# Kernel tuning notes

Measured on AMD Instinct MI355X. Metric: run time of the kernel, lower is better.

## Reference

```python
import jax, jax.numpy as jnp
import numpy as np

# Dimensions: B batch, V variables per sample, VT table rows, F feature, E embed_dim,
# NH healpix adjacency width. N6/N5/N4 grid sizes per zoom; PF fine patch points.
B, V, VT, F, E, NH = 2, 4, 4, 128, 128, 7
N6, N5, N4 = 196608, 49152, 12288
PF = 32768
P5, P4 = PF // 4, PF // 16   # coarse patch sizes
O5, O4 = 4, 16               # fine points per coarse point (4**(zoom - zoom_proc))
BIG = 1e10
EPS = 1e-20


def setup_inputs() -> dict:
    key = jax.random.key(0)
    ks = jax.random.split(key, 13)
    return {
        "table6": jax.random.normal(ks[0], (VT, N6, F), jnp.float32) * 0.02,
        "table5": jax.random.normal(ks[1], (VT, N5, F), jnp.float32) * 0.02,
        "table4": jax.random.normal(ks[2], (VT, N4, F), jnp.float32) * 0.02,
        "W": jax.random.normal(ks[3], (F, E), jnp.float32) / np.float32(np.sqrt(F)),
        "b": jnp.zeros((E,), jnp.float32),
        "rel_dists5": jax.random.uniform(ks[4], (B, P5, O5, NH), jnp.float32, 0.01, 1.0),
        "rel_dists4": jax.random.uniform(ks[5], (B, P4, O4, NH), jnp.float32, 0.01, 1.0),
        "mask5": (jax.random.uniform(ks[6], (B, P5, NH)) < 0.05).astype(jnp.float32),
        "mask4": (jax.random.uniform(ks[7], (B, P4, NH)) < 0.05).astype(jnp.float32),
        "var_indices": jax.random.randint(ks[8], (B, V), 0, VT),
        "idx6": jax.random.randint(ks[9], (B, PF), 0, N6),
        "nh_idx5": jax.random.randint(ks[10], (B, P5 * NH), 0, N5),
        "nh_idx4": jax.random.randint(ks[11], (B, P4 * NH), 0, N4),
    }


def _gather(table, var_idx, idx):
    # Fused get_embeddings_from_var_idx + get_patch / get_patch_nh:
    # out[b, v, p, f] = table[var_idx[b, v], idx[b, p], f]  -> [B, V, P, F]
    return table[var_idx[:, :, None], idx[:, None, :]]


def _interpolate(e, rel_dists, mask, n_out):
    # Embedding_interpolator: distance-weighted nh interpolation.
    # e: [B, V, Pc*NH, F]; rel_dists: [B, Pc, n_out, NH]; mask: [B, Pc, NH]
    rd = rel_dists + mask[:, :, None, :] * BIG  # invalid neighbors -> ~zero weight
    w = 1.0 / (EPS + rd)
    w = w / w.sum(axis=-1, keepdims=True)       # [B, Pc, n_out, NH]
    bsz, v, _, f = e.shape
    pc = rel_dists.shape[1]
    e = e.reshape(bsz, v, pc, NH, f)
    out = jnp.einsum('bvpnf,bpon->bvpof', e, w)  # [B, V, Pc, n_out, F]
    return out.reshape(bsz, v, 1, pc * n_out, f)  # t-dim unsqueezed, [B,V,1,PF,F]


def reference(table6, table5, table4, W, b, rel_dists5, rel_dists4,
              mask5, mask4, var_indices, idx6, nh_idx5, nh_idx4):
    # zoom_proc == zoom (6): patch gather + linear layer
    e6 = _gather(table6, var_indices, idx6)          # [B, V, PF, F]
    e6 = (e6 @ W + b)[:, :, None, :, :]              # [B, V, 1, PF, E]
    # zoom_proc 5 < zoom: nh gather + polar-distance interpolation (4 fine per coarse)
    e5 = _interpolate(_gather(table5, var_indices, nh_idx5), rel_dists5, mask5, O5)
    # zoom_proc 4 < zoom: nh gather + interpolation (16 fine per coarse)
    e4 = _interpolate(_gather(table4, var_indices, nh_idx4), rel_dists4, mask4, O4)
    return e6 + e5 + e4                               # [B, V, 1, PF, E]
```

## Files before the change

### kernel.cpp

```cpp
#include <hip/hip_runtime.h>
#include <cstdint>
#include <cstddef>

#define Bb 2
#define Vv 4
#define VTt 4
#define Ff 128
#define Ee 128
#define NHh 7
#define N6c 196608
#define N5c 49152
#define N4c 12288
#define PFc 32768
#define P5c 8192
#define P4c 2048
#define O5c 4
#define O4c 16
#define GRP 4

typedef __attribute__((ext_vector_type(8))) short short8;
typedef __attribute__((ext_vector_type(4))) float f32x4;
typedef __attribute__((ext_vector_type(4))) int i32x4;
typedef unsigned short u16;

__device__ __forceinline__ u16 f2bf(float f){
  union { float f; unsigned int i; } c; c.f = f;
  unsigned int x = c.i;
  return (u16)((x + 0x7fffu + ((x >> 16) & 1u)) >> 16);
}

__global__ void setup_kernel(const float* __restrict__ W, u16* __restrict__ wsw){
  int tid = blockIdx.x * 256 + threadIdx.x;
  if (tid < 16384){
    int j = tid & 7, lane = (tid >> 3) & 63, kk = (tid >> 9) & 3, nt = tid >> 11;
    int f = kk * 32 + (lane >> 4) * 8 + j;
    int e = nt * 16 + (lane & 15);
    wsw[tid] = f2bf(W[f * Ee + e]);
  }
}

__launch_bounds__(256, 2)
__global__ void mg_kernel(
    const float* __restrict__ t6, const float* __restrict__ t5, const float* __restrict__ t4,
    const float* __restrict__ rel5, const float* __restrict__ rel4,
    const float* __restrict__ m5, const float* __restrict__ m4,
    const int* __restrict__ vidx, const int* __restrict__ idx6,
    const int* __restrict__ nh5, const int* __restrict__ nh4,
    const u16* __restrict__ wsw, const float* __restrict__ bias,
    float* __restrict__ out)
{
  __shared__ float sT5[28 * 132];
  __shared__ float sT4[7 * 132];
  __shared__ float sW5[16 * 8];
  __shared__ float sW4[16 * 8];
  __shared__ float sB[Ee];
  __shared__ float sOut[16 * 132];

  const int tid = threadIdx.x;
  const int lane = tid & 63;
  const int wid = tid >> 6;
  const int blk = blockIdx.x;
  const int bv = blk / (P4c / GRP);
  const int pbase = (blk % (P4c / GRP)) * GRP;
  const int v = bv % Vv, b = bv / Vv;
  const int vi = vidx[b * Vv + v];

  if (tid < Ee) sB[tid] = bias[tid];

  short8 bfrag[2][4];
  const int ntb = wid * 2;
#pragma unroll
  for (int i = 0; i < 2; i++)
#pragma unroll
    for (int kk = 0; kk < 4; kk++)
      bfrag[i][kk] = *(const short8*)(wsw + (((ntb + i) * 4 + kk) * 64 + lane) * 8);

  const int m = lane & 15, q = lane >> 4;

  for (int g = 0; g < GRP; g++){
    const int pc4 = pbase + g;

    for (int k = tid; k < 896; k += 256){
      int row = k >> 5, c = k & 31;
      int gi = nh5[b * (P5c * NHh) + (pc4 * 4 + row / 7) * NHh + (row % 7)];
      *(f32x4*)(sT5 + row * 132 + c * 4) =
          *((const f32x4*)(t5 + ((size_t)vi * N5c + gi) * Ff) + c);
    }
    if (tid < 224){
      int row = tid >> 5, c = tid & 31;
      int gi = nh4[b * (P4c * NHh) + pc4 * NHh + row];
      *(f32x4*)(sT4 + row * 132 + c * 4) =
          *((const f32x4*)(t4 + ((size_t)vi * N4c + gi) * Ff) + c);
    }
    if (tid >= 128 && tid < 144){
      int t = tid - 128;
      float raw[7], s = 0.f;
#pragma unroll
      for (int n = 0; n < 7; n++){
        float rd = rel4[((b * P4c + pc4) * O4c + t) * NHh + n]
                 + m4[(b * P4c + pc4) * NHh + n] * 1e10f;
        raw[n] = 1.0f / (1e-20f + rd); s += raw[n];
      }
      float inv = 1.0f / s;
#pragma unroll
      for (int n = 0; n < 7; n++) sW4[t * 8 + n] = raw[n] * inv;
    } else if (tid >= 144 && tid < 160){
      int t = tid - 144;
      int pc5 = pc4 * 4 + (t >> 2), o = t & 3;
      float raw[7], s = 0.f;
#pragma unroll
      for (int n = 0; n < 7; n++){
        float rd = rel5[((b * P5c + pc5) * O5c + o) * NHh + n]
                 + m5[(b * P5c + pc5) * NHh + n] * 1e10f;
        raw[n] = 1.0f / (1e-20f + rd); s += raw[n];
      }
      float inv = 1.0f / s;
#pragma unroll
      for (int n = 0; n < 7; n++) sW5[t * 8 + n] = raw[n] * inv;
    }

    int rown = idx6[b * PFc + pc4 * 16 + m];
    const float* arow = t6 + ((size_t)vi * N6c + rown) * Ff + q * 8;
    short8 af[4];
#pragma unroll
    for (int kk = 0; kk < 4; kk++){
      f32x4 lo = *(const f32x4*)(arow + kk * 32);
      f32x4 hi = *(const f32x4*)(arow + kk * 32 + 4);
      short8 t;
#pragma unroll
      for (int j = 0; j < 4; j++){
        t[j]     = (short)f2bf(lo[j]);
        t[j + 4] = (short)f2bf(hi[j]);
      }
      af[kk] = t;
    }

    f32x4 acc0 = {0.f, 0.f, 0.f, 0.f}, acc1 = {0.f, 0.f, 0.f, 0.f};
#pragma unroll
    for (int kk = 0; kk < 4; kk++){
      acc0 = __builtin_amdgcn_mfma_f32_16x16x32_bf16(af[kk], bfrag[0][kk], acc0, 0, 0, 0);
      acc1 = __builtin_amdgcn_mfma_f32_16x16x32_bf16(af[kk], bfrag[1][kk], acc1, 0, 0, 0);
    }

    __syncthreads();

    for (int k = tid; k < 1024; k += 256){
      int t = k >> 6, ep = (k & 63) * 2;
      float v0 = sB[ep], v1 = sB[ep + 1];
      int r5 = (t >> 2) * 7;
      const float* w4p = sW4 + t * 8;
      const float* w5p = sW5 + t * 8;
#pragma unroll
      for (int n = 0; n < 7; n++){
        const float* p4 = sT4 + n * 132 + ep;
        float w4 = w4p[n];
        v0 += w4 * p4[0];
        v1 += w4 * p4[1];
        const float* p5 = sT5 + (r5 + n) * 132 + ep;
        float w5 = w5p[n];
        v0 += w5 * p5[0];
        v1 += w5 * p5[1];
      }
      sOut[t * 132 + ep] = v0;
      sOut[t * 132 + ep + 1] = v1;
    }

    __syncthreads();

    {
      int col = wid * 32 + m;
#pragma unroll
      for (int r = 0; r < 4; r++){
        int row = q * 4 + r;
        sOut[row * 132 + col]      += acc0[r];
        sOut[row * 132 + col + 16] += acc1[r];
      }
    }

    __syncthreads();

    {
      int t = tid >> 4, c = (tid & 15) * 8;
      const float* sp = sOut + t * 132 + c;
      size_t obase = (((size_t)bv) * PFc + (size_t)pc4 * 16 + t) * Ee + c;
      *(f32x4*)(out + obase)     = *(const f32x4*)(sp);
      *(f32x4*)(out + obase + 4) = *(const f32x4*)(sp + 4);
    }
  }
}

extern "C" void kernel_launch(void* const* d_in, const int* in_sizes, int n_in,
                              void* d_out, int out_size, void* d_ws, size_t ws_size,
                              hipStream_t stream){
  const float* t6   = (const float*)d_in[0];
  const float* t5   = (const float*)d_in[1];
  const float* t4   = (const float*)d_in[2];
  const float* W    = (const float*)d_in[3];
  const float* bias = (const float*)d_in[4];
  const float* rel5 = (const float*)d_in[5];
  const float* rel4 = (const float*)d_in[6];
  const float* m5   = (const float*)d_in[7];
  const float* m4   = (const float*)d_in[8];
  const int* vidx = (const int*)d_in[9];
  const int* idx6 = (const int*)d_in[10];
  const int* nh5  = (const int*)d_in[11];
  const int* nh4  = (const int*)d_in[12];

  u16* wsw = (u16*)d_ws;

  setup_kernel<<<64, 256, 0, stream>>>(W, wsw);

  int grid = (Bb * Vv * P4c) / GRP;
  mg_kernel<<<grid, 256, 0, stream>>>(t6, t5, t4, rel5, rel4, m5, m4,
                                      vidx, idx6, nh5, nh4, wsw, bias,
                                      (float*)d_out);
}
```

Before: 703.7 us.

## Double-buffer neighbor gathers via direct global-to-LDS loads and overlap with compute

Neighbor rows for zoom 5 and 4 are now loaded with global_load_lds straight into a double-buffered shared array. The next group's gather is issued before the current group's MFMA and interpolation work. The __syncthreads calls become custom waitcnt+barrier macros, occupancy is raised to 3 blocks per SM, LDS reads are vectorized to float2, and output stores are nontemporal. LDS rows lose their padding, which may cause bank conflicts. The barrier at the top of each group waits on all outstanding vector memory operations, and this may limit how much of the prefetch actually overlaps.

```diff
diff --git a/kernel.cpp b/kernel.cpp
--- a/kernel.cpp
+++ b/kernel.cpp
@@ -20,7 +20,7 @@
 
 typedef __attribute__((ext_vector_type(8))) short short8;
 typedef __attribute__((ext_vector_type(4))) float f32x4;
-typedef __attribute__((ext_vector_type(4))) int i32x4;
+typedef __attribute__((ext_vector_type(2))) float f32x2;
 typedef unsigned short u16;
 
 __device__ __forceinline__ u16 f2bf(float f){
@@ -39,7 +39,16 @@
   }
 }
 
-__launch_bounds__(256, 2)
+__device__ __forceinline__ void gload_lds16(const float* g, float* l){
+  __builtin_amdgcn_global_load_lds(
+      (const __attribute__((address_space(1))) unsigned int*)g,
+      (__attribute__((address_space(3))) unsigned int*)l, 16, 0, 0);
+}
+
+#define BAR_CONSUME() asm volatile("s_waitcnt vmcnt(0) lgkmcnt(0)\n\ts_barrier" ::: "memory")
+#define BAR_LDS()     asm volatile("s_waitcnt lgkmcnt(0)\n\ts_barrier" ::: "memory")
+
+__launch_bounds__(256, 3)
 __global__ void mg_kernel(
     const float* __restrict__ t6, const float* __restrict__ t5, const float* __restrict__ t4,
     const float* __restrict__ rel5, const float* __restrict__ rel4,
@@ -49,8 +58,8 @@
     const u16* __restrict__ wsw, const float* __restrict__ bias,
     float* __restrict__ out)
 {
-  __shared__ float sT5[28 * 132];
-  __shared__ float sT4[7 * 132];
+  __shared__ float sT5[2][28 * 128];
+  __shared__ float sT4[2][7 * 128];
   __shared__ float sW5[16 * 8];
   __shared__ float sW4[16 * 8];
   __shared__ float sB[Ee];
@@ -67,6 +76,22 @@
 
   if (tid < Ee) sB[tid] = bias[tid];
 
+  auto stage = [&](int pp, int buf){
+    float* d5 = sT5[buf];
+    for (int k = tid; k < 896; k += 256){
+      int row = k >> 5, c = k & 31;
+      int gi = nh5[b * (P5c * NHh) + (pp * 4 + row / 7) * NHh + (row % 7)];
+      gload_lds16(t5 + ((size_t)vi * N5c + gi) * Ff + c * 4, d5 + k * 4);
+    }
+    if (tid < 224){
+      int row = tid >> 5, c = tid & 31;
+      int gi = nh4[b * (P4c * NHh) + pp * NHh + row];
+      gload_lds16(t4 + ((size_t)vi * N4c + gi) * Ff + c * 4, sT4[buf] + tid * 4);
+    }
+  };
+
+  stage(pbase, 0);
+
   short8 bfrag[2][4];
   const int ntb = wid * 2;
 #pragma unroll
@@ -79,19 +104,10 @@
 
   for (int g = 0; g < GRP; g++){
     const int pc4 = pbase + g;
-
-    for (int k = tid; k < 896; k += 256){
-      int row = k >> 5, c = k & 31;
-      int gi = nh5[b * (P5c * NHh) + (pc4 * 4 + row / 7) * NHh + (row % 7)];
-      *(f32x4*)(sT5 + row * 132 + c * 4) =
-          *((const f32x4*)(t5 + ((size_t)vi * N5c + gi) * Ff) + c);
-    }
-    if (tid < 224){
-      int row = tid >> 5, c = tid & 31;
-      int gi = nh4[b * (P4c * NHh) + pc4 * NHh + row];
-      *(f32x4*)(sT4 + row * 132 + c * 4) =
-          *((const f32x4*)(t4 + ((size_t)vi * N4c + gi) * Ff) + c);
-    }
+    const int cur = g & 1;
+    const float* sT5c = sT5[cur];
+    const float* sT4c = sT4[cur];
+
     if (tid >= 128 && tid < 144){
       int t = tid - 128;
       float raw[7], s = 0.f;
@@ -126,14 +142,18 @@
     for (int kk = 0; kk < 4; kk++){
       f32x4 lo = *(const f32x4*)(arow + kk * 32);
       f32x4 hi = *(const f32x4*)(arow + kk * 32 + 4);
-      short8 t;
+      short8 cv;
 #pragma unroll
       for (int j = 0; j < 4; j++){
-        t[j]     = (short)f2bf(lo[j]);
-        t[j + 4] = (short)f2bf(hi[j]);
-      }
-      af[kk] = t;
-    }
+        cv[j]     = (short)f2bf(lo[j]);
+        cv[j + 4] = (short)f2bf(hi[j]);
+      }
+      af[kk] = cv;
+    }
+
+    BAR_CONSUME();
+
+    if (g + 1 < GRP) stage(pc4 + 1, cur ^ 1);
 
     f32x4 acc0 = {0.f, 0.f, 0.f, 0.f}, acc1 = {0.f, 0.f, 0.f, 0.f};
 #pragma unroll
@@ -142,30 +162,27 @@
       acc1 = __builtin_amdgcn_mfma_f32_16x16x32_bf16(af[kk], bfrag[1][kk], acc1, 0, 0, 0);
     }
 
-    __syncthreads();
-
     for (int k = tid; k < 1024; k += 256){
       int t = k >> 6, ep = (k & 63) * 2;
       float v0 = sB[ep], v1 = sB[ep + 1];
-      int r5 = (t >> 2) * 7;
       const float* w4p = sW4 + t * 8;
       const float* w5p = sW5 + t * 8;
+      const float* b4 = sT4c + ep;
+      const float* b5 = sT5c + (t >> 2) * 7 * 128 + ep;
 #pragma unroll
       for (int n = 0; n < 7; n++){
-        const float* p4 = sT4 + n * 132 + ep;
+        f32x2 a4 = *(const f32x2*)(b4 + n * 128);
         float w4 = w4p[n];
-        v0 += w4 * p4[0];
-        v1 += w4 * p4[1];
-        const float* p5 = sT5 + (r5 + n) * 132 + ep;
+        v0 += w4 * a4[0]; v1 += w4 * a4[1];
+        f32x2 a5 = *(const f32x2*)(b5 + n * 128);
         float w5 = w5p[n];
-        v0 += w5 * p5[0];
-        v1 += w5 * p5[1];
-      }
-      sOut[t * 132 + ep] = v0;
+        v0 += w5 * a5[0]; v1 += w5 * a5[1];
+      }
+      sOut[t * 132 + ep]     = v0;
       sOut[t * 132 + ep + 1] = v1;
     }
 
-    __syncthreads();
+    BAR_LDS();
 
     {
       int col = wid * 32 + m;
@@ -177,14 +194,16 @@
       }
     }
 
-    __syncthreads();
+    BAR_LDS();
 
     {
       int t = tid >> 4, c = (tid & 15) * 8;
       const float* sp = sOut + t * 132 + c;
       size_t obase = (((size_t)bv) * PFc + (size_t)pc4 * 16 + t) * Ee + c;
-      *(f32x4*)(out + obase)     = *(const f32x4*)(sp);
-      *(f32x4*)(out + obase + 4) = *(const f32x4*)(sp + 4);
+      f32x4 w0 = *(const f32x4*)(sp);
+      f32x4 w1 = *(const f32x4*)(sp + 4);
+      __builtin_nontemporal_store(w0, (f32x4*)(out + obase));
+      __builtin_nontemporal_store(w1, (f32x4*)(out + obase + 4));
     }
   }
 }
```

Result: no change. 699.2 us (-0.6%).
